# Performance work log

Measured on AMD Instinct MI355X. Metric: run time of the kernel, lower is better.

## Reference

```python
import jax, jax.numpy as jnp
import numpy as np

TEMPERATURE = 0.5
EPS = 1e-12  # F.normalize eps


def setup_inputs() -> dict:
    key = jax.random.key(0)
    z = jax.random.normal(key, (2048, 8, 256), dtype=jnp.float32)
    return {"z": z}


def reference(z):
    B, D = z.shape[0], z.shape[1]
    z = z.reshape(B, D, -1)  # [B, D, F]
    # F.normalize along features
    norm = jnp.linalg.norm(z, axis=-1, keepdims=True)
    zn = z / jnp.maximum(norm, EPS)

    # Positive term: per sample b, sim among D views -> [B, D, D], off-diagonal sum
    sim_pos = jnp.exp(jnp.einsum('bdf,bef->bde', zn, zn) / TEMPERATURE)
    eye_d = jnp.eye(D, dtype=bool)
    pos = jnp.sum(jnp.where(eye_d[None], 0.0, sim_pos), axis=(1, 2))  # [B]

    # Negative term: per view d, sim among B samples -> [D, B, B], row-wise off-diag mean, summed over views
    sim_neg = jnp.exp(jnp.einsum('bdf,cdf->dbc', zn, zn) / TEMPERATURE)
    eye_b = jnp.eye(B, dtype=bool)
    neg = jnp.sum(jnp.where(eye_b[None], 0.0, sim_neg), axis=-1) / (B - 1)  # [D, B]
    neg = jnp.sum(neg, axis=0)  # [B]

    logits = pos / (pos + neg)  # [B]
    # torch CrossEntropyLoss(reduction='sum') with 1-D input [C] and float target ones(C):
    # loss = -sum_c target_c * log_softmax(logits)_c = -sum(log_softmax(logits))
    error = -jnp.sum(jax.nn.log_softmax(logits))
    return error / B
```

## Files before the change

### kernel.cpp

```cpp
#include <hip/hip_runtime.h>
#include <hip/hip_bf16.h>

#define B_N 2048
#define D_V 8
#define F_D 256
#define TILE 128
#define BC 64
#define LSTR 264

typedef __attribute__((ext_vector_type(8))) short short8;
typedef __attribute__((ext_vector_type(4))) float floatx4;

__device__ inline unsigned short f2bf(float f) {
    __hip_bfloat16 h = __float2bfloat16(f);
    return *reinterpret_cast<unsigned short*>(&h);
}

__device__ inline float wave_reduce_sum(float v) {
    #pragma unroll
    for (int off = 1; off < 64; off <<= 1)
        v += __shfl_xor(v, off, 64);
    return v;
}

__global__ void norm_kernel(const float* __restrict__ z,
                            unsigned short* __restrict__ zn,
                            float* __restrict__ ns8) {
    int gid = blockIdx.x * blockDim.x + threadIdx.x;
    if (gid < D_V * B_N) ns8[gid] = 0.0f;
    int wave = gid >> 6;
    int lane = threadIdx.x & 63;
    const float4* zp = (const float4*)(z + (size_t)wave * F_D);
    float4 v = zp[lane];
    float ss = v.x * v.x + v.y * v.y + v.z * v.z + v.w * v.w;
    ss = wave_reduce_sum(ss);
    float inv = 1.0f / fmaxf(sqrtf(ss), 1e-12f);
    int b = wave >> 3, d = wave & 7;
    unsigned short* op = zn + (size_t)d * (B_N * F_D) + (size_t)b * F_D + lane * 4;
    ushort4 o;
    o.x = f2bf(v.x * inv);
    o.y = f2bf(v.y * inv);
    o.z = f2bf(v.z * inv);
    o.w = f2bf(v.w * inv);
    *(ushort4*)op = o;
}

__global__ void pos_kernel(const unsigned short* __restrict__ zn,
                           float* __restrict__ pos) {
    int gw = (blockIdx.x * blockDim.x + threadIdx.x) >> 6;
    int lane = threadIdx.x & 63;
    int q = lane >> 4, li = lane & 15;
    int s0 = gw * 2;
    int b = s0 + (li >> 3), d = li & 7;
    const unsigned short* rowp = zn + (size_t)d * (B_N * F_D) + (size_t)b * F_D;
    short8 a[8];
    #pragma unroll
    for (int kk = 0; kk < 8; kk++)
        a[kk] = *(const short8*)(rowp + kk * 32 + q * 8);
    floatx4 acc = {0.f, 0.f, 0.f, 0.f};
    #pragma unroll
    for (int kk = 0; kk < 8; kk++)
        acc = __builtin_amdgcn_mfma_f32_16x16x32_bf16(a[kk], a[kk], acc, 0, 0, 0);
    float p0 = 0.f, p1 = 0.f;
    #pragma unroll
    for (int r = 0; r < 4; r++) {
        int row = q * 4 + r, col = li;
        bool same_sample = (row >> 3) == (col >> 3);
        if (same_sample && row != col) {
            float e = __expf(2.0f * acc[r]);
            if (row < 8) p0 += e; else p1 += e;
        }
    }
    p0 = wave_reduce_sum(p0);
    p1 = wave_reduce_sum(p1);
    if (lane == 0) { pos[s0] = p0; pos[s0 + 1] = p1; }
}

__global__ __launch_bounds__(128, 2)
void neg_kernel(const unsigned short* __restrict__ zn,
                float* __restrict__ ns8) {
    __shared__ __align__(16) unsigned short Bs[BC * LSTR];
    __shared__ float csred[2][TILE];
    const int d = blockIdx.y;
    int trem = blockIdx.x;
    int i = 0;
    while (trem >= 16 - i) { trem -= 16 - i; ++i; }
    const int j = i + trem;
    const bool diag = (i == j);
    const unsigned short* Z = zn + (size_t)d * (B_N * F_D);
    int tid = threadIdx.x, w = tid >> 6, lane = tid & 63;
    int q = lane >> 4, li = lane & 15;
    int r0 = i * TILE + w * 64;

    short8 a[4][8];
    #pragma unroll
    for (int s = 0; s < 4; s++)
        #pragma unroll
        for (int kk = 0; kk < 8; kk++)
            a[s][kk] = *(const short8*)(Z + (size_t)(r0 + s * 16 + li) * F_D + kk * 32 + q * 8);

    float rs[4][4];
    #pragma unroll
    for (int s = 0; s < 4; s++)
        #pragma unroll
        for (int r = 0; r < 4; r++) rs[s][r] = 0.f;
    float cacc[2] = {0.f, 0.f};

    for (int stage = 0; stage < 2; ++stage) {
        int c0 = j * TILE + stage * BC;
        __syncthreads();
        #pragma unroll
        for (int it = 0; it < 16; ++it) {
            int idx = it * 128 + tid;
            int row = idx >> 5, kc = idx & 31;
            *(short8*)(&Bs[row * LSTR + kc * 8]) =
                *(const short8*)(Z + (size_t)(c0 + row) * F_D + kc * 8);
        }
        __syncthreads();
        #pragma unroll
        for (int ct = 0; ct < 4; ++ct) {
            short8 bf[8];
            #pragma unroll
            for (int kk = 0; kk < 8; kk++)
                bf[kk] = *(const short8*)(&Bs[(ct * 16 + li) * LSTR + kk * 32 + q * 8]);
            floatx4 acc[4];
            #pragma unroll
            for (int s = 0; s < 4; s++) acc[s] = (floatx4){0.f, 0.f, 0.f, 0.f};
            #pragma unroll
            for (int kk = 0; kk < 8; kk++)
                #pragma unroll
                for (int s = 0; s < 4; s++)
                    acc[s] = __builtin_amdgcn_mfma_f32_16x16x32_bf16(a[s][kk], bf[kk], acc[s], 0, 0, 0);
            int gcol = c0 + ct * 16 + li;
            float csum = 0.f;
            #pragma unroll
            for (int s = 0; s < 4; s++) {
                #pragma unroll
                for (int r = 0; r < 4; r++) {
                    float e = __expf(2.0f * acc[s][r]);
                    int grow = r0 + s * 16 + q * 4 + r;
                    e = (diag && grow == gcol) ? 0.f : e;
                    rs[s][r] += e;
                    csum += e;
                }
            }
            csum += __shfl_xor(csum, 16, 64);
            csum += __shfl_xor(csum, 32, 64);
            if (q == ct) cacc[stage] += csum;
        }
    }

    #pragma unroll
    for (int off = 1; off < 16; off <<= 1)
        #pragma unroll
        for (int s = 0; s < 4; s++)
            #pragma unroll
            for (int r = 0; r < 4; r++)
                rs[s][r] += __shfl_xor(rs[s][r], off, 64);
    if (li == 0) {
        #pragma unroll
        for (int s = 0; s < 4; s++)
            #pragma unroll
            for (int r = 0; r < 4; r++)
                atomicAdd(&ns8[d * B_N + r0 + s * 16 + q * 4 + r], rs[s][r]);
    }

    csred[w][lane] = cacc[0];
    csred[w][64 + lane] = cacc[1];
    __syncthreads();
    if (!diag && tid < TILE) {
        float v = csred[0][tid] + csred[1][tid];
        atomicAdd(&ns8[d * B_N + j * TILE + tid], v);
    }
}

__global__ void final_kernel(const float* __restrict__ pos,
                             const float* __restrict__ ns8,
                             float* __restrict__ out) {
    __shared__ float red[256];
    int t = threadIdx.x;
    float vals[8];
    float lmax = -1e30f;
    #pragma unroll
    for (int i = 0; i < 8; i++) {
        int idx = t * 8 + i;
        float nsum = 0.f;
        #pragma unroll
        for (int d = 0; d < D_V; d++) nsum += ns8[d * B_N + idx];
        float p = pos[idx];
        float n = nsum * (1.0f / (float)(B_N - 1));
        float l = p / (p + n);
        vals[i] = l;
        lmax = fmaxf(lmax, l);
    }
    red[t] = lmax; __syncthreads();
    for (int s = 128; s > 0; s >>= 1) {
        if (t < s) red[t] = fmaxf(red[t], red[t + s]);
        __syncthreads();
    }
    float m = red[0]; __syncthreads();
    float se = 0.f, sl = 0.f;
    #pragma unroll
    for (int i = 0; i < 8; i++) { se += expf(vals[i] - m); sl += vals[i]; }
    red[t] = se; __syncthreads();
    for (int s = 128; s > 0; s >>= 1) {
        if (t < s) red[t] += red[t + s];
        __syncthreads();
    }
    float S = red[0]; __syncthreads();
    red[t] = sl; __syncthreads();
    for (int s = 128; s > 0; s >>= 1) {
        if (t < s) red[t] += red[t + s];
        __syncthreads();
    }
    if (t == 0) out[0] = m + logf(S) - red[0] / (float)B_N;
}

extern "C" void kernel_launch(void* const* d_in, const int* in_sizes, int n_in,
                              void* d_out, int out_size, void* d_ws, size_t ws_size,
                              hipStream_t stream) {
    const float* z = (const float*)d_in[0];
    float* out = (float*)d_out;
    unsigned short* zn = (unsigned short*)d_ws;
    float* ns8 = (float*)((char*)d_ws + (size_t)D_V * B_N * F_D * 2);
    float* pos = ns8 + D_V * B_N;

    norm_kernel<<<dim3(4096), 256, 0, stream>>>(z, zn, ns8);
    pos_kernel<<<dim3(256), 256, 0, stream>>>(zn, pos);
    neg_kernel<<<dim3(136, 8), 128, 0, stream>>>(zn, ns8);
    final_kernel<<<1, 256, 0, stream>>>(pos, ns8, out);
}
```

Baseline: 95.53 us.

## Fuse normalize with positive term, fold final reduction into last neg block

Merges the normalization and positive-similarity kernels into one kernel that keeps normalized rows in shared memory. The final log-softmax reduction moves into the last-finishing neg block through an atomic ticket counter, which removes two launches. The scale sqrt(2/ln2) is folded into the normalized vectors so the exponential becomes a bare exp2. Column sums in the neg kernel are now written by every lane with atomics instead of going through a shared buffer. The risks are bf16 rounding of the scaled values and the ordering that the threadfence and ticket scheme must guarantee.

```diff
diff --git a/kernel.cpp b/kernel.cpp
--- a/kernel.cpp
+++ b/kernel.cpp
@@ -8,6 +8,18 @@
 #define BC 64
 #define LSTR 264
 
+#define SCALE_F 1.69864364f
+
+#if defined(__has_builtin)
+#  if __has_builtin(__builtin_amdgcn_exp2f)
+#    define EXP2F(x) __builtin_amdgcn_exp2f(x)
+#  else
+#    define EXP2F(x) exp2f(x)
+#  endif
+#else
+#  define EXP2F(x) exp2f(x)
+#endif
+
 typedef __attribute__((ext_vector_type(8))) short short8;
 typedef __attribute__((ext_vector_type(4))) float floatx4;
 
@@ -23,66 +35,83 @@
     return v;
 }
 
-__global__ void norm_kernel(const float* __restrict__ z,
-                            unsigned short* __restrict__ zn,
-                            float* __restrict__ ns8) {
-    int gid = blockIdx.x * blockDim.x + threadIdx.x;
+__device__ inline float wave_reduce_max(float v) {
+    #pragma unroll
+    for (int off = 1; off < 64; off <<= 1)
+        v = fmaxf(v, __shfl_xor(v, off, 64));
+    return v;
+}
+
+__global__ __launch_bounds__(256)
+void np_kernel(const float* __restrict__ z, unsigned short* __restrict__ zn,
+               float* __restrict__ ns8, float* __restrict__ pos,
+               unsigned int* __restrict__ cnt) {
+    __shared__ __align__(16) unsigned short Zs[32 * LSTR];
+    int tid = threadIdx.x;
+    int gid = blockIdx.x * 256 + tid;
     if (gid < D_V * B_N) ns8[gid] = 0.0f;
-    int wave = gid >> 6;
-    int lane = threadIdx.x & 63;
-    const float4* zp = (const float4*)(z + (size_t)wave * F_D);
-    float4 v = zp[lane];
-    float ss = v.x * v.x + v.y * v.y + v.z * v.z + v.w * v.w;
-    ss = wave_reduce_sum(ss);
-    float inv = 1.0f / fmaxf(sqrtf(ss), 1e-12f);
-    int b = wave >> 3, d = wave & 7;
-    unsigned short* op = zn + (size_t)d * (B_N * F_D) + (size_t)b * F_D + lane * 4;
-    ushort4 o;
-    o.x = f2bf(v.x * inv);
-    o.y = f2bf(v.y * inv);
-    o.z = f2bf(v.z * inv);
-    o.w = f2bf(v.w * inv);
-    *(ushort4*)op = o;
-}
-
-__global__ void pos_kernel(const unsigned short* __restrict__ zn,
-                           float* __restrict__ pos) {
-    int gw = (blockIdx.x * blockDim.x + threadIdx.x) >> 6;
-    int lane = threadIdx.x & 63;
-    int q = lane >> 4, li = lane & 15;
-    int s0 = gw * 2;
-    int b = s0 + (li >> 3), d = li & 7;
-    const unsigned short* rowp = zn + (size_t)d * (B_N * F_D) + (size_t)b * F_D;
-    short8 a[8];
-    #pragma unroll
-    for (int kk = 0; kk < 8; kk++)
-        a[kk] = *(const short8*)(rowp + kk * 32 + q * 8);
-    floatx4 acc = {0.f, 0.f, 0.f, 0.f};
-    #pragma unroll
-    for (int kk = 0; kk < 8; kk++)
-        acc = __builtin_amdgcn_mfma_f32_16x16x32_bf16(a[kk], a[kk], acc, 0, 0, 0);
-    float p0 = 0.f, p1 = 0.f;
-    #pragma unroll
-    for (int r = 0; r < 4; r++) {
-        int row = q * 4 + r, col = li;
-        bool same_sample = (row >> 3) == (col >> 3);
-        if (same_sample && row != col) {
-            float e = __expf(2.0f * acc[r]);
-            if (row < 8) p0 += e; else p1 += e;
-        }
-    }
-    p0 = wave_reduce_sum(p0);
-    p1 = wave_reduce_sum(p1);
-    if (lane == 0) { pos[s0] = p0; pos[s0 + 1] = p1; }
+    if (gid == 0) *cnt = 0u;
+
+    int w = tid >> 6, lane = tid & 63;
+    int b = blockIdx.x * 4 + w;
+    #pragma unroll
+    for (int k = 0; k < 8; k++) {
+        const float4 v = ((const float4*)(z + ((size_t)b * 8 + k) * F_D))[lane];
+        float ss = v.x * v.x + v.y * v.y + v.z * v.z + v.w * v.w;
+        ss = wave_reduce_sum(ss);
+        float inv = SCALE_F / fmaxf(sqrtf(ss), 1e-12f);
+        ushort4 o;
+        o.x = f2bf(v.x * inv);
+        o.y = f2bf(v.y * inv);
+        o.z = f2bf(v.z * inv);
+        o.w = f2bf(v.w * inv);
+        ((ushort4*)(zn + (size_t)k * (B_N * F_D) + (size_t)b * F_D))[lane] = o;
+        *(ushort4*)(&Zs[(w * 8 + k) * LSTR + lane * 4]) = o;
+    }
+    __syncthreads();
+
+    if (w < 2) {
+        int q = lane >> 4, li = lane & 15;
+        int lr = (w * 2 + (li >> 3)) * 8 + (li & 7);
+        short8 a[8];
+        #pragma unroll
+        for (int kk = 0; kk < 8; kk++)
+            a[kk] = *(const short8*)(&Zs[lr * LSTR + kk * 32 + q * 8]);
+        floatx4 acc = {0.f, 0.f, 0.f, 0.f};
+        #pragma unroll
+        for (int kk = 0; kk < 8; kk++)
+            acc = __builtin_amdgcn_mfma_f32_16x16x32_bf16(a[kk], a[kk], acc, 0, 0, 0);
+        float p0 = 0.f, p1 = 0.f;
+        #pragma unroll
+        for (int r = 0; r < 4; r++) {
+            int row = q * 4 + r, col = li;
+            bool same_sample = (row >> 3) == (col >> 3);
+            if (same_sample && row != col) {
+                float e = EXP2F(acc[r]);
+                if (row < 8) p0 += e; else p1 += e;
+            }
+        }
+        p0 = wave_reduce_sum(p0);
+        p1 = wave_reduce_sum(p1);
+        if (lane == 0) {
+            int s0 = blockIdx.x * 4 + w * 2;
+            pos[s0] = p0;
+            pos[s0 + 1] = p1;
+        }
+    }
 }
 
 __global__ __launch_bounds__(128, 2)
 void neg_kernel(const unsigned short* __restrict__ zn,
-                float* __restrict__ ns8) {
+                float* __restrict__ ns8,
+                const float* __restrict__ pos,
+                float* __restrict__ out,
+                unsigned int* __restrict__ cnt) {
     __shared__ __align__(16) unsigned short Bs[BC * LSTR];
-    __shared__ float csred[2][TILE];
-    const int d = blockIdx.y;
-    int trem = blockIdx.x;
+    __shared__ unsigned int tk_s;
+    const int bid = blockIdx.x;
+    const int d = bid & 7;
+    int trem = bid >> 3;
     int i = 0;
     while (trem >= 16 - i) { trem -= 16 - i; ++i; }
     const int j = i + trem;
@@ -104,8 +133,9 @@
     for (int s = 0; s < 4; s++)
         #pragma unroll
         for (int r = 0; r < 4; r++) rs[s][r] = 0.f;
-    float cacc[2] = {0.f, 0.f};
-
+    float cs[8];
+
+    #pragma unroll
     for (int stage = 0; stage < 2; ++stage) {
         int c0 = j * TILE + stage * BC;
         __syncthreads();
@@ -137,16 +167,16 @@
             for (int s = 0; s < 4; s++) {
                 #pragma unroll
                 for (int r = 0; r < 4; r++) {
-                    float e = __expf(2.0f * acc[s][r]);
-                    int grow = r0 + s * 16 + q * 4 + r;
-                    e = (diag && grow == gcol) ? 0.f : e;
+                    float e = EXP2F(acc[s][r]);
+                    if (diag) {
+                        int grow = r0 + s * 16 + q * 4 + r;
+                        if (grow == gcol) e = 0.f;
+                    }
                     rs[s][r] += e;
                     csum += e;
                 }
             }
-            csum += __shfl_xor(csum, 16, 64);
-            csum += __shfl_xor(csum, 32, 64);
-            if (q == ct) cacc[stage] += csum;
+            cs[stage * 4 + ct] = csum;
         }
     }
 
@@ -157,63 +187,67 @@
             #pragma unroll
             for (int r = 0; r < 4; r++)
                 rs[s][r] += __shfl_xor(rs[s][r], off, 64);
-    if (li == 0) {
+    {
+        float rv = 0.f;
         #pragma unroll
         for (int s = 0; s < 4; s++)
             #pragma unroll
             for (int r = 0; r < 4; r++)
-                atomicAdd(&ns8[d * B_N + r0 + s * 16 + q * 4 + r], rs[s][r]);
-    }
-
-    csred[w][lane] = cacc[0];
-    csred[w][64 + lane] = cacc[1];
-    __syncthreads();
-    if (!diag && tid < TILE) {
-        float v = csred[0][tid] + csred[1][tid];
-        atomicAdd(&ns8[d * B_N + j * TILE + tid], v);
-    }
-}
-
-__global__ void final_kernel(const float* __restrict__ pos,
-                             const float* __restrict__ ns8,
-                             float* __restrict__ out) {
-    __shared__ float red[256];
-    int t = threadIdx.x;
-    float vals[8];
+                if (li == s * 4 + r) rv = rs[s][r];
+        int grow = r0 + (li >> 2) * 16 + q * 4 + (li & 3);
+        atomicAdd(&ns8[d * B_N + grow], rv);
+    }
+
+    if (!diag) {
+        #pragma unroll
+        for (int c = 0; c < 8; c++) {
+            cs[c] += __shfl_xor(cs[c], 16, 64);
+            cs[c] += __shfl_xor(cs[c], 32, 64);
+        }
+        float v0 = 0.f, v1 = 0.f;
+        #pragma unroll
+        for (int c = 0; c < 4; c++)
+            if (q == c) { v0 = cs[c]; v1 = cs[c + 4]; }
+        atomicAdd(&ns8[d * B_N + j * TILE + q * 16 + li], v0);
+        atomicAdd(&ns8[d * B_N + j * TILE + 64 + q * 16 + li], v1);
+    }
+
+    __threadfence();
+    if (tid == 0) tk_s = atomicAdd(cnt, 1u);
+    __syncthreads();
+    if (tk_s != gridDim.x - 1) return;
+    __threadfence();
+
+    float* fr = (float*)Bs;
+    float vals[16];
     float lmax = -1e30f;
     #pragma unroll
-    for (int i = 0; i < 8; i++) {
-        int idx = t * 8 + i;
+    for (int t2 = 0; t2 < 16; t2++) {
+        int idx = t2 * 128 + tid;
         float nsum = 0.f;
         #pragma unroll
-        for (int d = 0; d < D_V; d++) nsum += ns8[d * B_N + idx];
+        for (int dd = 0; dd < D_V; dd++) nsum += ns8[dd * B_N + idx];
         float p = pos[idx];
-        float n = nsum * (1.0f / (float)(B_N - 1));
-        float l = p / (p + n);
-        vals[i] = l;
+        float l = p / (p + nsum * (1.0f / (float)(B_N - 1)));
+        vals[t2] = l;
         lmax = fmaxf(lmax, l);
     }
-    red[t] = lmax; __syncthreads();
-    for (int s = 128; s > 0; s >>= 1) {
-        if (t < s) red[t] = fmaxf(red[t], red[t + s]);
-        __syncthreads();
-    }
-    float m = red[0]; __syncthreads();
+    lmax = wave_reduce_max(lmax);
+    if (lane == 0) fr[w] = lmax;
+    __syncthreads();
+    float m = fmaxf(fr[0], fr[1]);
     float se = 0.f, sl = 0.f;
     #pragma unroll
-    for (int i = 0; i < 8; i++) { se += expf(vals[i] - m); sl += vals[i]; }
-    red[t] = se; __syncthreads();
-    for (int s = 128; s > 0; s >>= 1) {
-        if (t < s) red[t] += red[t + s];
-        __syncthreads();
-    }
-    float S = red[0]; __syncthreads();
-    red[t] = sl; __syncthreads();
-    for (int s = 128; s > 0; s >>= 1) {
-        if (t < s) red[t] += red[t + s];
-        __syncthreads();
-    }
-    if (t == 0) out[0] = m + logf(S) - red[0] / (float)B_N;
+    for (int t2 = 0; t2 < 16; t2++) {
+        se += expf(vals[t2] - m);
+        sl += vals[t2];
+    }
+    se = wave_reduce_sum(se);
+    sl = wave_reduce_sum(sl);
+    if (lane == 0) { fr[2 + w] = se; fr[6 + w] = sl; }
+    __syncthreads();
+    if (tid == 0)
+        out[0] = m + logf(fr[2] + fr[3]) - (fr[6] + fr[7]) * (1.0f / (float)B_N);
 }
 
 extern "C" void kernel_launch(void* const* d_in, const int* in_sizes, int n_in,
@@ -224,9 +258,8 @@
     unsigned short* zn = (unsigned short*)d_ws;
     float* ns8 = (float*)((char*)d_ws + (size_t)D_V * B_N * F_D * 2);
     float* pos = ns8 + D_V * B_N;
-
-    norm_kernel<<<dim3(4096), 256, 0, stream>>>(z, zn, ns8);
-    pos_kernel<<<dim3(256), 256, 0, stream>>>(zn, pos);
-    neg_kernel<<<dim3(136, 8), 128, 0, stream>>>(zn, ns8);
-    final_kernel<<<1, 256, 0, stream>>>(pos, ns8, out);
-}
+    unsigned int* cnt = (unsigned int*)(pos + B_N);
+
+    np_kernel<<<dim3(512), 256, 0, stream>>>(z, zn, ns8, pos, cnt);
+    neg_kernel<<<dim3(1088), 128, 0, stream>>>(zn, ns8, pos, out, cnt);
+}
```

Result: slower. 135.6 us (+41.9%).

## Fold exp scale into normalization, use exp2, and split neg tile over four waves

Applied to the files above, without the earlier changes.

The normalized vectors are pre-scaled by sqrt(2/ln2), so each dot product already equals the exponent in base 2 and a raw exp2 builtin replaces the scaled exp. The neg kernel now runs 256 threads (four waves of 32 rows each) instead of two waves of 64 rows, which halves per-thread A registers and accumulators and should raise occupancy. B fragments are streamed per kk instead of held as eight registers. Column sums are kept per lane and reduced once at the end, dropping the shared-memory column reduction and one barrier, and the LDS row stride changes from 264 to 258. Rounding the pre-scaled values to bf16 changes the rounding slightly, and the 258 stride may break 16-byte alignment of short8 LDS accesses.

```diff
diff --git a/kernel.cpp b/kernel.cpp
--- a/kernel.cpp
+++ b/kernel.cpp
@@ -6,7 +6,19 @@
 #define F_D 256
 #define TILE 128
 #define BC 64
-#define LSTR 264
+#define LSTR 258
+
+#define SCALE_F 1.69864364f
+
+#if defined(__has_builtin)
+#  if __has_builtin(__builtin_amdgcn_exp2f)
+#    define EXP2F(x) __builtin_amdgcn_exp2f(x)
+#  else
+#    define EXP2F(x) exp2f(x)
+#  endif
+#else
+#  define EXP2F(x) exp2f(x)
+#endif
 
 typedef __attribute__((ext_vector_type(8))) short short8;
 typedef __attribute__((ext_vector_type(4))) float floatx4;
@@ -34,7 +46,7 @@
     float4 v = zp[lane];
     float ss = v.x * v.x + v.y * v.y + v.z * v.z + v.w * v.w;
     ss = wave_reduce_sum(ss);
-    float inv = 1.0f / fmaxf(sqrtf(ss), 1e-12f);
+    float inv = SCALE_F / fmaxf(sqrtf(ss), 1e-12f);
     int b = wave >> 3, d = wave & 7;
     unsigned short* op = zn + (size_t)d * (B_N * F_D) + (size_t)b * F_D + lane * 4;
     ushort4 o;
@@ -67,7 +79,7 @@
         int row = q * 4 + r, col = li;
         bool same_sample = (row >> 3) == (col >> 3);
         if (same_sample && row != col) {
-            float e = __expf(2.0f * acc[r]);
+            float e = EXP2F(acc[r]);
             if (row < 8) p0 += e; else p1 += e;
         }
     }
@@ -76,11 +88,10 @@
     if (lane == 0) { pos[s0] = p0; pos[s0 + 1] = p1; }
 }
 
-__global__ __launch_bounds__(128, 2)
+__global__ __launch_bounds__(256)
 void neg_kernel(const unsigned short* __restrict__ zn,
                 float* __restrict__ ns8) {
     __shared__ __align__(16) unsigned short Bs[BC * LSTR];
-    __shared__ float csred[2][TILE];
     const int d = blockIdx.y;
     int trem = blockIdx.x;
     int i = 0;
@@ -90,28 +101,29 @@
     const unsigned short* Z = zn + (size_t)d * (B_N * F_D);
     int tid = threadIdx.x, w = tid >> 6, lane = tid & 63;
     int q = lane >> 4, li = lane & 15;
-    int r0 = i * TILE + w * 64;
-
-    short8 a[4][8];
-    #pragma unroll
-    for (int s = 0; s < 4; s++)
+    int r0 = i * TILE + w * 32;
+
+    short8 a[2][8];
+    #pragma unroll
+    for (int s = 0; s < 2; s++)
         #pragma unroll
         for (int kk = 0; kk < 8; kk++)
             a[s][kk] = *(const short8*)(Z + (size_t)(r0 + s * 16 + li) * F_D + kk * 32 + q * 8);
 
-    float rs[4][4];
-    #pragma unroll
-    for (int s = 0; s < 4; s++)
+    float rs[2][4];
+    #pragma unroll
+    for (int s = 0; s < 2; s++)
         #pragma unroll
         for (int r = 0; r < 4; r++) rs[s][r] = 0.f;
-    float cacc[2] = {0.f, 0.f};
-
+    float cs[8];
+
+    #pragma unroll
     for (int stage = 0; stage < 2; ++stage) {
         int c0 = j * TILE + stage * BC;
         __syncthreads();
         #pragma unroll
-        for (int it = 0; it < 16; ++it) {
-            int idx = it * 128 + tid;
+        for (int it = 0; it < 8; ++it) {
+            int idx = it * 256 + tid;
             int row = idx >> 5, kc = idx & 31;
             *(short8*)(&Bs[row * LSTR + kc * 8]) =
                 *(const short8*)(Z + (size_t)(c0 + row) * F_D + kc * 8);
@@ -119,58 +131,65 @@
         __syncthreads();
         #pragma unroll
         for (int ct = 0; ct < 4; ++ct) {
-            short8 bf[8];
-            #pragma unroll
-            for (int kk = 0; kk < 8; kk++)
-                bf[kk] = *(const short8*)(&Bs[(ct * 16 + li) * LSTR + kk * 32 + q * 8]);
-            floatx4 acc[4];
-            #pragma unroll
-            for (int s = 0; s < 4; s++) acc[s] = (floatx4){0.f, 0.f, 0.f, 0.f};
-            #pragma unroll
-            for (int kk = 0; kk < 8; kk++)
-                #pragma unroll
-                for (int s = 0; s < 4; s++)
-                    acc[s] = __builtin_amdgcn_mfma_f32_16x16x32_bf16(a[s][kk], bf[kk], acc[s], 0, 0, 0);
+            const unsigned short* bp = &Bs[(ct * 16 + li) * LSTR + q * 8];
+            floatx4 acc[2];
+            acc[0] = (floatx4){0.f, 0.f, 0.f, 0.f};
+            acc[1] = (floatx4){0.f, 0.f, 0.f, 0.f};
+            #pragma unroll
+            for (int kk = 0; kk < 8; kk++) {
+                short8 bf = *(const short8*)(bp + kk * 32);
+                acc[0] = __builtin_amdgcn_mfma_f32_16x16x32_bf16(a[0][kk], bf, acc[0], 0, 0, 0);
+                acc[1] = __builtin_amdgcn_mfma_f32_16x16x32_bf16(a[1][kk], bf, acc[1], 0, 0, 0);
+            }
             int gcol = c0 + ct * 16 + li;
             float csum = 0.f;
             #pragma unroll
-            for (int s = 0; s < 4; s++) {
+            for (int s = 0; s < 2; s++) {
                 #pragma unroll
                 for (int r = 0; r < 4; r++) {
-                    float e = __expf(2.0f * acc[s][r]);
-                    int grow = r0 + s * 16 + q * 4 + r;
-                    e = (diag && grow == gcol) ? 0.f : e;
+                    float e = EXP2F(acc[s][r]);
+                    if (diag) {
+                        int grow = r0 + s * 16 + q * 4 + r;
+                        if (grow == gcol) e = 0.f;
+                    }
                     rs[s][r] += e;
                     csum += e;
                 }
             }
-            csum += __shfl_xor(csum, 16, 64);
-            csum += __shfl_xor(csum, 32, 64);
-            if (q == ct) cacc[stage] += csum;
+            cs[stage * 4 + ct] = csum;
         }
     }
 
     #pragma unroll
     for (int off = 1; off < 16; off <<= 1)
         #pragma unroll
-        for (int s = 0; s < 4; s++)
+        for (int s = 0; s < 2; s++)
             #pragma unroll
             for (int r = 0; r < 4; r++)
                 rs[s][r] += __shfl_xor(rs[s][r], off, 64);
-    if (li == 0) {
-        #pragma unroll
-        for (int s = 0; s < 4; s++)
+    {
+        float rv = 0.f;
+        #pragma unroll
+        for (int s = 0; s < 2; s++)
             #pragma unroll
             for (int r = 0; r < 4; r++)
-                atomicAdd(&ns8[d * B_N + r0 + s * 16 + q * 4 + r], rs[s][r]);
-    }
-
-    csred[w][lane] = cacc[0];
-    csred[w][64 + lane] = cacc[1];
-    __syncthreads();
-    if (!diag && tid < TILE) {
-        float v = csred[0][tid] + csred[1][tid];
-        atomicAdd(&ns8[d * B_N + j * TILE + tid], v);
+                if (li == s * 4 + r) rv = rs[s][r];
+        if (li < 8)
+            atomicAdd(&ns8[d * B_N + r0 + (li >> 2) * 16 + q * 4 + (li & 3)], rv);
+    }
+
+    if (!diag) {
+        #pragma unroll
+        for (int c = 0; c < 8; c++) {
+            cs[c] += __shfl_xor(cs[c], 16, 64);
+            cs[c] += __shfl_xor(cs[c], 32, 64);
+        }
+        float v0 = 0.f, v1 = 0.f;
+        #pragma unroll
+        for (int c = 0; c < 4; c++)
+            if (q == c) { v0 = cs[c]; v1 = cs[c + 4]; }
+        atomicAdd(&ns8[d * B_N + j * TILE + q * 16 + li], v0);
+        atomicAdd(&ns8[d * B_N + j * TILE + 64 + q * 16 + li], v1);
     }
 }
 
@@ -227,6 +246,6 @@
 
     norm_kernel<<<dim3(4096), 256, 0, stream>>>(z, zn, ns8);
     pos_kernel<<<dim3(256), 256, 0, stream>>>(zn, pos);
-    neg_kernel<<<dim3(136, 8), 128, 0, stream>>>(zn, ns8);
+    neg_kernel<<<dim3(136, 8), 256, 0, stream>>>(zn, ns8);
     final_kernel<<<1, 256, 0, stream>>>(pos, ns8, out);
 }
```

Result: slower. 135.9 us (+42.3%).
